# Kernel optimization log

Measured on AMD Instinct MI355X. Metric: run time of the kernel, lower is better.

## Reference

```python
import jax, jax.numpy as jnp
import numpy as np

N = 100000
E = 1600000
D = 128   # path_code_size
H = 32    # GIN hidden dim (hard-coded in module)
BN_EPS = 1e-5
GIN_EPS = 0.0  # GINConv default eps


def gin_conv(x, src, dst, Wa, ba, Wb, bb, num_nodes):
    # sum-aggregate neighbor features: messages x[src] scattered to dst
    agg = jax.ops.segment_sum(x[src], dst, num_segments=num_nodes)
    h = (1.0 + GIN_EPS) * x + agg
    h = jax.nn.relu(h @ Wa + ba)
    return h @ Wb + bb


def batch_norm(x, gamma, beta):
    # training-mode BN over the node dimension (biased variance, like torch)
    mean = jnp.mean(x, axis=0)
    var = jnp.mean((x - mean) ** 2, axis=0)
    return (x - mean) * jax.lax.rsqrt(var + BN_EPS) * gamma + beta


def setup_inputs() -> dict:
    key = jax.random.key(0)
    ks = jax.random.split(key, 12)
    x = jax.random.normal(ks[0], (N, D), dtype=jnp.float32)
    edge_index = jax.random.randint(ks[1], (2, E), 0, N, dtype=jnp.int64)

    def lin(k, fan_in, fan_out):
        bound = 1.0 / np.sqrt(fan_in)
        kw, kb = jax.random.split(k)
        W = jax.random.uniform(kw, (fan_in, fan_out), jnp.float32, -bound, bound)
        b = jax.random.uniform(kb, (fan_out,), jnp.float32, -bound, bound)
        return W, b

    W1a, b1a = lin(ks[2], D, H)
    W1b, b1b = lin(ks[3], H, H)
    W2a, b2a = lin(ks[4], H, H)
    W2b, b2b = lin(ks[5], H, D)
    return {
        "x": x, "edge_index": edge_index,
        "W1a": W1a, "b1a": b1a, "W1b": W1b, "b1b": b1b,
        "g1": jnp.ones((H,), jnp.float32), "be1": jnp.zeros((H,), jnp.float32),
        "W2a": W2a, "b2a": b2a, "W2b": W2b, "b2b": b2b,
        "g2": jnp.ones((D,), jnp.float32), "be2": jnp.zeros((D,), jnp.float32),
    }


def reference(x, edge_index, W1a, b1a, W1b, b1b, g1, be1, W2a, b2a, W2b, b2b, g2, be2):
    src, dst = edge_index[0], edge_index[1]
    h = jax.nn.relu(gin_conv(x, src, dst, W1a, b1a, W1b, b1b, N))
    h = batch_norm(h, g1, be1)
    h = jax.nn.relu(gin_conv(h, src, dst, W2a, b2a, W2b, b2b, N))
    h = batch_norm(h, g2, be2)
    return h
```

## Files before the change

### kernel.cpp

```cpp
#include <hip/hip_runtime.h>

constexpr int NN  = 100000;
constexpr int NE  = 1600000;
constexpr int D   = 128;
constexpr int H   = 32;
constexpr int CAP = 64;
constexpr int NTILE = 4;
constexpr int TILE_SZ = NN / NTILE;


__global__ __launch_bounds__(256) void k_fill(const int* __restrict__ src,
                                              const int* __restrict__ dst,
                                              int* __restrict__ cnt,
                                              int* __restrict__ slots) {
    for (int e = blockIdx.x * blockDim.x + threadIdx.x; e < NE;
         e += gridDim.x * blockDim.x) {
        const int d = dst[e];
        const int pos = atomicAdd(&cnt[d], 1);
        if (pos < CAP) slots[d * CAP + pos] = src[e];
    }
}

__global__ __launch_bounds__(256) void k_xw1(const float* __restrict__ x,
                                             const float* __restrict__ W,
                                             float* __restrict__ z) {
    __shared__ float Wl[D * H];
    for (int i = threadIdx.x; i < D * H; i += blockDim.x) Wl[i] = W[i];
    __syncthreads();
    const int j = threadIdx.x & 31;
    const int g = threadIdx.x >> 5;
    const int groups = blockDim.x >> 5;
    for (int n = blockIdx.x * groups + g; n < NN; n += gridDim.x * groups) {
        const float* xr = x + (size_t)n * D;
        float acc = 0.f;
#pragma unroll 8
        for (int k = 0; k < D; ++k) acc = fmaf(xr[k], Wl[k * H + j], acc);
        z[n * H + j] = acc;
    }
}

__global__ __launch_bounds__(256) void k_gather(const float* __restrict__ z,
                                                const int* __restrict__ cnt,
                                                const int* __restrict__ slots,
                                                float* __restrict__ agg,
                                                int lo, int first) {
    const int j = threadIdx.x & 31;
    const int g = threadIdx.x >> 5;
    const int groups = blockDim.x >> 5;
    for (int n = blockIdx.x * groups + g; n < NN; n += gridDim.x * groups) {
        const int deg = min(cnt[n], CAP);
        const int* row = slots + n * CAP;
        float t = 0.f;
        for (int e = 0; e < deg; e += 8) {
            const int4 a = *(const int4*)(row + e);
            const int4 b = *(const int4*)(row + e + 4);
            if ((unsigned)(a.x - lo) < (unsigned)TILE_SZ)                 t += z[a.x * H + j];
            if (e + 1 < deg && (unsigned)(a.y - lo) < (unsigned)TILE_SZ)  t += z[a.y * H + j];
            if (e + 2 < deg && (unsigned)(a.z - lo) < (unsigned)TILE_SZ)  t += z[a.z * H + j];
            if (e + 3 < deg && (unsigned)(a.w - lo) < (unsigned)TILE_SZ)  t += z[a.w * H + j];
            if (e + 4 < deg && (unsigned)(b.x - lo) < (unsigned)TILE_SZ)  t += z[b.x * H + j];
            if (e + 5 < deg && (unsigned)(b.y - lo) < (unsigned)TILE_SZ)  t += z[b.y * H + j];
            if (e + 6 < deg && (unsigned)(b.z - lo) < (unsigned)TILE_SZ)  t += z[b.z * H + j];
            if (e + 7 < deg && (unsigned)(b.w - lo) < (unsigned)TILE_SZ)  t += z[b.w * H + j];
        }
        float* ap = agg + (size_t)n * H + j;
        if (first) {
            __builtin_nontemporal_store(t, ap);
        } else {
            __builtin_nontemporal_store(t + *ap, ap);
        }
    }
}

__global__ __launch_bounds__(256) void k_mlp1(const float* __restrict__ z,
                                              float* __restrict__ buf,
                                              const float* __restrict__ b1a,
                                              const float* __restrict__ W1b,
                                              const float* __restrict__ b1b,
                                              float* __restrict__ gsum,
                                              float* __restrict__ gsq) {
    __shared__ float Wl[H * H];
    __shared__ float lsum[H], lsq[H];
    for (int i = threadIdx.x; i < H * H; i += blockDim.x) Wl[i] = W1b[i];
    if (threadIdx.x < H) { lsum[threadIdx.x] = 0.f; lsq[threadIdx.x] = 0.f; }
    __syncthreads();
    const int j = threadIdx.x & 31;
    const int g = threadIdx.x >> 5;
    const int groups = blockDim.x >> 5;
    const float ba = b1a[j], bb = b1b[j];
    float psum = 0.f, psq = 0.f;
    for (int n = blockIdx.x * groups + g; n < NN; n += gridDim.x * groups) {
        float t = z[n * H + j] + buf[n * H + j] + ba;
        t = fmaxf(t, 0.f);
        float u = bb;
#pragma unroll
        for (int k = 0; k < H; ++k) u = fmaf(__shfl(t, k, 32), Wl[k * H + j], u);
        const float r = fmaxf(u, 0.f);
        buf[n * H + j] = r;
        psum += r;
        psq = fmaf(r, r, psq);
    }
    atomicAdd(&lsum[j], psum);
    atomicAdd(&lsq[j], psq);
    __syncthreads();
    if (threadIdx.x < H) {
        atomicAdd(&gsum[threadIdx.x], lsum[threadIdx.x]);
        atomicAdd(&gsq[threadIdx.x], lsq[threadIdx.x]);
    }
}

__global__ void k_finalize(const float* __restrict__ gsum, const float* __restrict__ gsq,
                           const float* __restrict__ gamma, const float* __restrict__ beta,
                           float* __restrict__ scale, float* __restrict__ shift, int C) {
    const int j = threadIdx.x;
    if (j < C) {
        const float mean = gsum[j] * (1.f / NN);
        const float var  = gsq[j] * (1.f / NN) - mean * mean;
        const float sc   = gamma[j] * rsqrtf(var + 1e-5f);
        scale[j] = sc;
        shift[j] = beta[j] - mean * sc;
    }
}

__global__ __launch_bounds__(256) void k_bn_w2a(const float* __restrict__ r1,
                                                const float* __restrict__ scale,
                                                const float* __restrict__ shift,
                                                const float* __restrict__ W2a,
                                                float* __restrict__ z2) {
    __shared__ float Wl[H * H];
    for (int i = threadIdx.x; i < H * H; i += blockDim.x) Wl[i] = W2a[i];
    __syncthreads();
    const int j = threadIdx.x & 31;
    const int g = threadIdx.x >> 5;
    const int groups = blockDim.x >> 5;
    const float sc = scale[j], sh = shift[j];
    for (int n = blockIdx.x * groups + g; n < NN; n += gridDim.x * groups) {
        const float y = fmaf(r1[n * H + j], sc, sh);
        float u = 0.f;
#pragma unroll
        for (int k = 0; k < H; ++k) u = fmaf(__shfl(y, k, 32), Wl[k * H + j], u);
        z2[n * H + j] = u;
    }
}

__global__ __launch_bounds__(256) void k_mlp2(const float* __restrict__ z2,
                                              const float* __restrict__ agg,
                                              const float* __restrict__ b2a,
                                              const float* __restrict__ W2b,
                                              const float* __restrict__ b2b,
                                              float* __restrict__ out,
                                              float* __restrict__ gsum,
                                              float* __restrict__ gsq) {
    __shared__ float Wl[H * D];
    __shared__ float lsum[D], lsq[D];
    for (int i = threadIdx.x; i < H * D; i += blockDim.x) Wl[i] = W2b[i];
    if (threadIdx.x < D) { lsum[threadIdx.x] = 0.f; lsq[threadIdx.x] = 0.f; }
    __syncthreads();
    const int lane = threadIdx.x & 63;
    const int wid  = threadIdx.x >> 6;
    const int j    = lane & 31;
    const float ba  = b2a[j];
    const float bb0 = b2b[lane], bb1 = b2b[64 + lane];
    float ps0 = 0.f, pq0 = 0.f, ps1 = 0.f, pq1 = 0.f;
    const int nw = (gridDim.x * blockDim.x) >> 6;
    for (int n = blockIdx.x * 4 + wid; n < NN; n += nw) {
        float t = z2[(size_t)n * H + j] + agg[(size_t)n * H + j] + ba;
        t = fmaxf(t, 0.f);
        float u0 = bb0, u1 = bb1;
#pragma unroll
        for (int k = 0; k < H; ++k) {
            const float tk = __shfl(t, k, 32);
            u0 = fmaf(tk, Wl[k * D + lane], u0);
            u1 = fmaf(tk, Wl[k * D + 64 + lane], u1);
        }
        const float r0 = fmaxf(u0, 0.f), r1v = fmaxf(u1, 0.f);
        out[(size_t)n * D + lane]      = r0;
        out[(size_t)n * D + 64 + lane] = r1v;
        ps0 += r0;  pq0 = fmaf(r0, r0, pq0);
        ps1 += r1v; pq1 = fmaf(r1v, r1v, pq1);
    }
    atomicAdd(&lsum[lane], ps0);      atomicAdd(&lsq[lane], pq0);
    atomicAdd(&lsum[64 + lane], ps1); atomicAdd(&lsq[64 + lane], pq1);
    __syncthreads();
    if (threadIdx.x < D) {
        atomicAdd(&gsum[threadIdx.x], lsum[threadIdx.x]);
        atomicAdd(&gsq[threadIdx.x], lsq[threadIdx.x]);
    }
}

__global__ __launch_bounds__(256) void k_bn_out(float* __restrict__ out,
                                                const float* __restrict__ scale,
                                                const float* __restrict__ shift) {
    const int total = NN * D / 4;
    float4* o4 = (float4*)out;
    for (int i = blockIdx.x * blockDim.x + threadIdx.x; i < total;
         i += gridDim.x * blockDim.x) {
        float4 v = o4[i];
        const int c = (i & 31) * 4;
        v.x = fmaf(v.x, scale[c + 0], shift[c + 0]);
        v.y = fmaf(v.y, scale[c + 1], shift[c + 1]);
        v.z = fmaf(v.z, scale[c + 2], shift[c + 2]);
        v.w = fmaf(v.w, scale[c + 3], shift[c + 3]);
        o4[i] = v;
    }
}

extern "C" void kernel_launch(void* const* d_in, const int* in_sizes, int n_in,
                              void* d_out, int out_size, void* d_ws, size_t ws_size,
                              hipStream_t stream) {
    const float* x   = (const float*)d_in[0];
    const int*   ei  = (const int*)d_in[1];
    const float* W1a = (const float*)d_in[2];
    const float* b1a = (const float*)d_in[3];
    const float* W1b = (const float*)d_in[4];
    const float* b1b = (const float*)d_in[5];
    const float* g1  = (const float*)d_in[6];
    const float* be1 = (const float*)d_in[7];
    const float* W2a = (const float*)d_in[8];
    const float* b2a = (const float*)d_in[9];
    const float* W2b = (const float*)d_in[10];
    const float* b2b = (const float*)d_in[11];
    const float* g2  = (const float*)d_in[12];
    const float* be2 = (const float*)d_in[13];
    float* out = (float*)d_out;
    const int* src = ei;
    const int* dst = ei + NE;

    float* ws = (float*)d_ws;
    float* z    = ws;
    float* buf  = ws + (size_t)NN * H;
    int*   cnt  = (int*)(ws + 2 * (size_t)NN * H);
    float* st   = ws + 2 * (size_t)NN * H + NN;
    int*   slots = (int*)(st + 640);
    float* gsum1 = st;        float* gsq1 = st + 32;
    float* sc1   = st + 64;   float* sh1  = st + 96;
    float* gsum2 = st + 128;  float* gsq2 = st + 256;
    float* sc2   = st + 384;  float* sh2  = st + 512;

    hipMemsetAsync(cnt, 0, (NN + 640) * sizeof(float), stream);

    k_fill<<<2048, 256, 0, stream>>>(src, dst, cnt, slots);

    k_xw1<<<2048, 256, 0, stream>>>(x, W1a, z);
    for (int t = 0; t < NTILE; ++t)
        k_gather<<<2048, 256, 0, stream>>>(z, cnt, slots, buf, t * TILE_SZ, t == 0);
    k_mlp1<<<2048, 256, 0, stream>>>(z, buf, b1a, W1b, b1b, gsum1, gsq1);
    k_finalize<<<1, 128, 0, stream>>>(gsum1, gsq1, g1, be1, sc1, sh1, H);

    k_bn_w2a<<<2048, 256, 0, stream>>>(buf, sc1, sh1, W2a, z);
    for (int t = 0; t < NTILE; ++t)
        k_gather<<<2048, 256, 0, stream>>>(z, cnt, slots, buf, t * TILE_SZ, t == 0);
    k_mlp2<<<2048, 256, 0, stream>>>(z, buf, b2a, W2b, b2b, out, gsum2, gsq2);
    k_finalize<<<1, 128, 0, stream>>>(gsum2, gsq2, g2, be2, sc2, sh2, D);
    k_bn_out<<<2048, 256, 0, stream>>>(out, sc2, sh2);
}
```

Before: 702.7 us.

## Replace CSR-slot gather aggregation with per-edge atomic scatter-add

Drops the slot-table build (atomic counters plus a capped 64-slot adjacency list) and the four tiled gather passes. Each GIN aggregation becomes one kernel in which each thread takes one (edge, feature) pair and atomically adds z[src] into agg[dst], after a memset of the accumulator. This removes the preprocessing kernel and the tiling passes, but costs 51M float atomics per layer with contention on popular destinations. Summation order is also nondeterministic. It does fix the silent truncation of nodes with degree above 64.

```diff
diff --git a/kernel.cpp b/kernel.cpp
--- a/kernel.cpp
+++ b/kernel.cpp
@@ -4,20 +4,20 @@
 constexpr int NE  = 1600000;
 constexpr int D   = 128;
 constexpr int H   = 32;
-constexpr int CAP = 64;
-constexpr int NTILE = 4;
-constexpr int TILE_SZ = NN / NTILE;
-
-
-__global__ __launch_bounds__(256) void k_fill(const int* __restrict__ src,
-                                              const int* __restrict__ dst,
-                                              int* __restrict__ cnt,
-                                              int* __restrict__ slots) {
-    for (int e = blockIdx.x * blockDim.x + threadIdx.x; e < NE;
-         e += gridDim.x * blockDim.x) {
+
+
+__global__ __launch_bounds__(256) void k_scatter(const int* __restrict__ src,
+                                                 const int* __restrict__ dst,
+                                                 const float* __restrict__ z,
+                                                 float* __restrict__ agg) {
+    const int total = NE * H;
+    for (int i = blockIdx.x * blockDim.x + threadIdx.x; i < total;
+         i += gridDim.x * blockDim.x) {
+        const int e = i >> 5;
+        const int f = i & 31;
+        const int s = src[e];
         const int d = dst[e];
-        const int pos = atomicAdd(&cnt[d], 1);
-        if (pos < CAP) slots[d * CAP + pos] = src[e];
+        atomicAdd(&agg[d * H + f], z[s * H + f]);
     }
 }
 
@@ -36,39 +36,6 @@
 #pragma unroll 8
         for (int k = 0; k < D; ++k) acc = fmaf(xr[k], Wl[k * H + j], acc);
         z[n * H + j] = acc;
-    }
-}
-
-__global__ __launch_bounds__(256) void k_gather(const float* __restrict__ z,
-                                                const int* __restrict__ cnt,
-                                                const int* __restrict__ slots,
-                                                float* __restrict__ agg,
-                                                int lo, int first) {
-    const int j = threadIdx.x & 31;
-    const int g = threadIdx.x >> 5;
-    const int groups = blockDim.x >> 5;
-    for (int n = blockIdx.x * groups + g; n < NN; n += gridDim.x * groups) {
-        const int deg = min(cnt[n], CAP);
-        const int* row = slots + n * CAP;
-        float t = 0.f;
-        for (int e = 0; e < deg; e += 8) {
-            const int4 a = *(const int4*)(row + e);
-            const int4 b = *(const int4*)(row + e + 4);
-            if ((unsigned)(a.x - lo) < (unsigned)TILE_SZ)                 t += z[a.x * H + j];
-            if (e + 1 < deg && (unsigned)(a.y - lo) < (unsigned)TILE_SZ)  t += z[a.y * H + j];
-            if (e + 2 < deg && (unsigned)(a.z - lo) < (unsigned)TILE_SZ)  t += z[a.z * H + j];
-            if (e + 3 < deg && (unsigned)(a.w - lo) < (unsigned)TILE_SZ)  t += z[a.w * H + j];
-            if (e + 4 < deg && (unsigned)(b.x - lo) < (unsigned)TILE_SZ)  t += z[b.x * H + j];
-            if (e + 5 < deg && (unsigned)(b.y - lo) < (unsigned)TILE_SZ)  t += z[b.y * H + j];
-            if (e + 6 < deg && (unsigned)(b.z - lo) < (unsigned)TILE_SZ)  t += z[b.z * H + j];
-            if (e + 7 < deg && (unsigned)(b.w - lo) < (unsigned)TILE_SZ)  t += z[b.w * H + j];
-        }
-        float* ap = agg + (size_t)n * H + j;
-        if (first) {
-            __builtin_nontemporal_store(t, ap);
-        } else {
-            __builtin_nontemporal_store(t + *ap, ap);
-        }
     }
 }
 
@@ -226,30 +193,25 @@
     const int* src = ei;
     const int* dst = ei + NE;
 
-    float* ws = (float*)d_ws;
-    float* z    = ws;
-    float* buf  = ws + (size_t)NN * H;
-    int*   cnt  = (int*)(ws + 2 * (size_t)NN * H);
-    float* st   = ws + 2 * (size_t)NN * H + NN;
-    int*   slots = (int*)(st + 640);
+    float* ws  = (float*)d_ws;
+    float* z   = ws;
+    float* buf = ws + (size_t)NN * H;
+    float* st  = ws + 2 * (size_t)NN * H;
     float* gsum1 = st;        float* gsq1 = st + 32;
     float* sc1   = st + 64;   float* sh1  = st + 96;
     float* gsum2 = st + 128;  float* gsq2 = st + 256;
     float* sc2   = st + 384;  float* sh2  = st + 512;
 
-    hipMemsetAsync(cnt, 0, (NN + 640) * sizeof(float), stream);
-
-    k_fill<<<2048, 256, 0, stream>>>(src, dst, cnt, slots);
-
+    hipMemsetAsync(buf, 0, (size_t)NN * H * sizeof(float) + 640 * sizeof(float),
+                   stream);
     k_xw1<<<2048, 256, 0, stream>>>(x, W1a, z);
-    for (int t = 0; t < NTILE; ++t)
-        k_gather<<<2048, 256, 0, stream>>>(z, cnt, slots, buf, t * TILE_SZ, t == 0);
+    k_scatter<<<4096, 256, 0, stream>>>(src, dst, z, buf);
     k_mlp1<<<2048, 256, 0, stream>>>(z, buf, b1a, W1b, b1b, gsum1, gsq1);
     k_finalize<<<1, 128, 0, stream>>>(gsum1, gsq1, g1, be1, sc1, sh1, H);
 
     k_bn_w2a<<<2048, 256, 0, stream>>>(buf, sc1, sh1, W2a, z);
-    for (int t = 0; t < NTILE; ++t)
-        k_gather<<<2048, 256, 0, stream>>>(z, cnt, slots, buf, t * TILE_SZ, t == 0);
+    hipMemsetAsync(buf, 0, (size_t)NN * H * sizeof(float), stream);
+    k_scatter<<<4096, 256, 0, stream>>>(src, dst, z, buf);
     k_mlp2<<<2048, 256, 0, stream>>>(z, buf, b2a, W2b, b2b, out, gsum2, gsq2);
     k_finalize<<<1, 128, 0, stream>>>(gsum2, gsq2, g2, be2, sc2, sh2, D);
     k_bn_out<<<2048, 256, 0, stream>>>(out, sc2, sh2);
```

After: 692.3 us. No clear change (-1.5%).
